# Kernel tuning notes

Measured on AMD Instinct MI355X. Metric: run time of the kernel, lower is better.

## Reference

```python
import jax, jax.numpy as jnp
import numpy as np

NH, DH, DHR = 16, 128, 64  # heads, head dim, decoupled rope dim
ROPE_BASE = 10000.0

def _rope(x):
    # x: (B, L, H, Dr) with Dr even; interleaved-pair RoPE (torchtune style)
    B, L, H, Dr = x.shape
    pos = jnp.arange(L, dtype=jnp.float32)
    inv_freq = 1.0 / (ROPE_BASE ** (jnp.arange(0, Dr, 2, dtype=jnp.float32) / Dr))
    ang = pos[:, None] * inv_freq[None, :]          # (L, Dr/2)
    cos = jnp.cos(ang)[None, :, None, :].astype(x.dtype)
    sin = jnp.sin(ang)[None, :, None, :].astype(x.dtype)
    x1, x2 = x[..., 0::2], x[..., 1::2]
    out = jnp.stack([x1 * cos - x2 * sin, x1 * sin + x2 * cos], axis=-1)
    return out.reshape(B, L, H, Dr)

def setup_inputs() -> dict:
    key = jax.random.key(0)
    ks = jax.random.split(key, 9)
    s = 0.02
    return {
        'x':     jax.random.normal(ks[0], (2, 2048, 2048), jnp.float32),
        'W_DKV': jax.random.normal(ks[1], (2048, 682), jnp.float32) * s,
        'W_UK':  jax.random.normal(ks[2], (682, 2048), jnp.float32) * s,
        'W_UV':  jax.random.normal(ks[3], (682, 2048), jnp.float32) * s,
        'W_KR':  jax.random.normal(ks[4], (2048, 64), jnp.float32) * s,
        'W_DQ':  jax.random.normal(ks[5], (2048, 682), jnp.float32) * s,
        'W_UQ':  jax.random.normal(ks[6], (682, 2048), jnp.float32) * s,
        'W_QR':  jax.random.normal(ks[7], (682, 1024), jnp.float32) * s,
        'W_O':   jax.random.normal(ks[8], (2048, 2048), jnp.float32) * s,
    }

def reference(x, W_DKV, W_UK, W_UV, W_KR, W_DQ, W_UQ, W_QR, W_O):
    B, L, D = x.shape
    # --- KV path ---
    c_KV = x @ W_DKV                                   # (B, L, dc)
    k_C = (c_KV @ W_UK).reshape(B, L, NH, DH)          # content keys
    k_R = _rope((x @ W_KR).reshape(B, L, 1, DHR))      # shared rope key head
    k_R = jnp.broadcast_to(k_R, (B, L, NH, DHR))
    k = jnp.concatenate([k_C, k_R], axis=-1)           # (B, L, NH, DH+DHR)
    v = (c_KV @ W_UV).reshape(B, L, NH, DH)
    # --- Q path ---
    c_Q = x @ W_DQ                                     # (B, L, dc')
    q_C = (c_Q @ W_UQ).reshape(B, L, NH, DH)
    q_R = _rope((c_Q @ W_QR).reshape(B, L, NH, DHR))
    q = jnp.concatenate([q_C, q_R], axis=-1)           # (B, L, NH, DH+DHR)
    # --- attention (causal) ---
    scale = 1.0 / jnp.sqrt(jnp.float32(DH + DHR))
    scores = jnp.einsum('blhd,bmhd->bhlm', q, k) * scale
    causal = jnp.tril(jnp.ones((L, L), dtype=bool))
    scores = jnp.where(causal[None, None], scores, jnp.finfo(scores.dtype).min)
    attn = jax.nn.softmax(scores, axis=-1)
    o = jnp.einsum('bhlm,bmhd->blhd', attn, v).reshape(B, L, NH * DH)
    return o @ W_O
```

## Files before the change

kernel.cpp:

```cpp
#include <hip/hip_runtime.h>
#include <stdint.h>

typedef __attribute__((ext_vector_type(8))) __bf16 bf16x8;
typedef __attribute__((ext_vector_type(4))) float f32x4;

#define DEVI static __device__ __forceinline__

DEVI uint16_t f2b(float f) {
  uint32_t u = __float_as_uint(f);
  u += 0x7FFFu + ((u >> 16) & 1u);
  return (uint16_t)(u >> 16);
}
DEVI float b2f(uint16_t b) { return __uint_as_float(((uint32_t)b) << 16); }

DEVI void gl_lds16(const void* g, void* l) {
  __builtin_amdgcn_global_load_lds((const __attribute__((address_space(1))) void*)g,
                                   (__attribute__((address_space(3))) void*)l, 16, 0, 0);
}

DEVI f32x4 mfma16(bf16x8 a, bf16x8 b, f32x4 c) {
  return __builtin_amdgcn_mfma_f32_16x16x32_bf16(a, b, c, 0, 0, 0);
}

#define BARX asm volatile("s_barrier" ::: "memory")
#define WLG0 asm volatile("s_waitcnt lgkmcnt(0)" ::: "memory")
#define WV4 asm volatile("s_waitcnt vmcnt(4)" ::: "memory")
#define PRIO1 __builtin_amdgcn_s_setprio(1)
#define PRIO0 __builtin_amdgcn_s_setprio(0)

static constexpr size_t OFF_XB = 0;
static constexpr size_t OFF_WD = 8388608;
static constexpr size_t OFF_WUKV = OFF_WD + 3670016;
static constexpr size_t OFF_WUQR = OFF_WUKV + 3145728;
static constexpr size_t OFF_WO = OFF_WUQR + 2359296;
static constexpr size_t OFF_CD = OFF_WO + 4194304;
static constexpr size_t OFF_CUKV = OFF_CD + 7340032;
static constexpr size_t OFF_CUQR = OFF_CUKV + 16777216;
static constexpr size_t OFF_VT = OFF_CUQR + 12582912;

__global__ void pre_kernel(const float* __restrict__ x, const float* __restrict__ Wdkv,
                           const float* __restrict__ Wuk, const float* __restrict__ Wuv,
                           const float* __restrict__ Wkr, const float* __restrict__ Wdq,
                           const float* __restrict__ Wuq, const float* __restrict__ Wqr,
                           const float* __restrict__ Wo, uint16_t* __restrict__ ws) {
  const int bid = blockIdx.x;
  const int t = threadIdx.x;
  if (bid >= 3264) {
    int id = (bid - 3264) * 256 + t;
    float4 v = ((const float4*)x)[id];
    uint16_t o[4] = {f2b(v.x), f2b(v.y), f2b(v.z), f2b(v.w)};
    *(uint64_t*)&ws[OFF_XB + (size_t)id * 4] = *(uint64_t*)o;
    return;
  }
  const float* W;
  uint16_t* Wt;
  int Kw, Nw, Kp, nx, rb;
  if (bid < 384) {
    W = Wdkv; Wt = ws + OFF_WD; Kw = 2048; Nw = 682; Kp = 2048; nx = 12; rb = bid;
  } else if (bid < 768) {
    W = Wdq; Wt = ws + OFF_WD + (size_t)768 * 2048; Kw = 2048; Nw = 682; Kp = 2048; nx = 12; rb = bid - 384;
  } else if (bid < 896) {
    W = Wkr; Wt = ws + OFF_WD + (size_t)1536 * 2048; Kw = 2048; Nw = 64; Kp = 2048; nx = 4; rb = bid - 768;
  } else if (bid < 1280) {
    W = Wuk; Wt = ws + OFF_WUKV; Kw = 682; Nw = 2048; Kp = 768; nx = 32; rb = bid - 896;
  } else if (bid < 1664) {
    W = Wuv; Wt = ws + OFF_WUKV + (size_t)2048 * 768; Kw = 682; Nw = 2048; Kp = 768; nx = 32; rb = bid - 1280;
  } else if (bid < 2048) {
    W = Wuq; Wt = ws + OFF_WUQR; Kw = 682; Nw = 2048; Kp = 768; nx = 32; rb = bid - 1664;
  } else if (bid < 2240) {
    W = Wqr; Wt = ws + OFF_WUQR + (size_t)2048 * 768; Kw = 682; Nw = 1024; Kp = 768; nx = 16; rb = bid - 2048;
  } else {
    W = Wo; Wt = ws + OFF_WO; Kw = 2048; Nw = 2048; Kp = 2048; nx = 32; rb = bid - 2240;
  }
  const int n0 = (rb % nx) * 64, k0 = (rb / nx) * 64;
  __shared__ uint16_t T[64][72];
#pragma unroll
  for (int p = 0; p < 2; ++p) {
    int r = p * 32 + (t >> 3);
    int c0 = (t & 7) * 8;
    int gr = k0 + r;
#pragma unroll
    for (int e = 0; e < 8; ++e) {
      int gc = n0 + c0 + e;
      float v = (gr < Kw && gc < Nw) ? W[(size_t)gr * Nw + gc] : 0.f;
      T[c0 + e][r] = f2b(v);
    }
  }
  __syncthreads();
#pragma unroll
  for (int p = 0; p < 2; ++p) {
    int dr = p * 32 + (t >> 3);
    int mc = (t & 7) * 8;
    uint16_t tmp[8];
#pragma unroll
    for (int e = 0; e < 8; ++e) tmp[e] = T[dr][mc + e];
    *(uint64_t*)&Wt[(size_t)(n0 + dr) * Kp + k0 + mc] = ((uint64_t*)tmp)[0];
    *(uint64_t*)&Wt[(size_t)(n0 + dr) * Kp + k0 + mc + 4] = ((uint64_t*)tmp)[1];
  }
}

template <int BM, bool F32OUT>
__global__ __launch_bounds__(512, 2) void gemm8(const uint16_t* __restrict__ A, int lda,
                                                const uint16_t* __restrict__ Bt,
                                                void* __restrict__ Cv, int ldc, int K) {
  constexpr int MF = BM / 32;
  constexpr int MH = MF / 2;
  constexpr int AL = BM / 128;
  constexpr int ABYTES = BM * 128;
  __shared__ char lds[2 * BM * 128 + 2 * 256 * 128];
  char* const LB = lds + 2 * ABYTES;
  const int tid = threadIdx.x;
  const int lane = tid & 63;
  const int lr = lane & 15, lgb = (lane >> 4) * 16;
  const int wid = tid >> 6;
  const int g = wid >> 2;
  const int wc = (wid & 3) * 64;
  const int rA0 = g * (BM / 2) + lr;
  const int rB0 = wc + lr;
  const size_t row0 = (size_t)blockIdx.y * BM, col0 = (size_t)blockIdx.x * 256;
  const char* Agb = (const char*)(A + row0 * lda);
  const char* Btb = (const char*)(Bt + col0 * K);
  const size_t ldab = (size_t)lda * 2;
  const size_t ldbb = (size_t)K * 2;
  const int nk = K >> 6;
  const int ni = nk >> 1;

  f32x4 acc[MF][4] = {};
  bf16x8 aF[MH][2], bF[4][2];

  auto stageA = [&](int kt, int buf, int hf) {
#pragma unroll
    for (int j = 0; j < AL; ++j) {
      int c = j * 512 + tid;
      int cl = c ^ (((c >> 5) & 1) << 1);
      int row = hf * (BM / 2) + (cl >> 3);
      gl_lds16(Agb + (size_t)row * ldab + (size_t)kt * 128 + (cl & 7) * 16,
               lds + buf * ABYTES + hf * (ABYTES / 2) + (j * 512 + (tid & 0x1C0)) * 16);
    }
  };
  auto stageB = [&](int kt, int buf, int hf) {
#pragma unroll
    for (int j = 0; j < 2; ++j) {
      int c = j * 512 + tid;
      int cl = c ^ (((c >> 5) & 1) << 1);
      int row = hf * 128 + (cl >> 3);
      gl_lds16(Btb + (size_t)row * ldbb + (size_t)kt * 128 + (cl & 7) * 16,
               LB + buf * 32768 + hf * 16384 + (j * 512 + (tid & 0x1C0)) * 16);
    }
  };
  auto ldAm = [&](int buf, int mb) {
#pragma unroll
    for (int m = 0; m < MH; ++m) {
      int r = rA0 + (mb + m) * 16;
      int ro = r * 128;
      int sw = ((r >> 2) & 1) << 5;
#pragma unroll
      for (int kk = 0; kk < 2; ++kk)
        aF[m][kk] = *(const bf16x8*)(lds + buf * ABYTES + ((ro + kk * 64 + lgb) ^ sw));
    }
  };
  auto ldBn = [&](int buf, int nb) {
#pragma unroll
    for (int n = 0; n < 2; ++n) {
      int r = rB0 + (nb + n) * 16;
      int ro = r * 128;
      int sw = ((r >> 2) & 1) << 5;
#pragma unroll
      for (int kk = 0; kk < 2; ++kk)
        bF[nb + n][kk] = *(const bf16x8*)(LB + buf * 32768 + ((ro + kk * 64 + lgb) ^ sw));
    }
  };
  auto mmac = [&](int mb, int nb) {
#pragma unroll
    for (int m = 0; m < MH; ++m)
#pragma unroll
      for (int n = 0; n < 2; ++n)
#pragma unroll
        for (int kk = 0; kk < 2; ++kk)
          acc[mb + m][nb + n] = mfma16(aF[m][kk], bF[nb + n][kk], acc[mb + m][nb + n]);
  };

  stageA(0, 0, 0); stageA(0, 0, 1); stageB(0, 0, 0); stageB(0, 0, 1);
  stageB(1, 1, 0); stageB(1, 1, 1);
  WV4; BARX;

  for (int i = 0; i < ni; ++i) {
    const int t1 = 2 * i + 1;
    const int tn = (2 * i + 2 < nk) ? 2 * i + 2 : nk - 1;
    const int tn1 = (2 * i + 3 < nk) ? 2 * i + 3 : nk - 1;
    ldAm(0, 0); ldBn(0, 0); stageA(t1, 1, 0);
    BARX; WLG0; PRIO1; mmac(0, 0); PRIO0; BARX;
    ldBn(0, 2); stageA(t1, 1, 1);
    BARX; WLG0; PRIO1; mmac(0, 2); PRIO0; BARX;
    ldAm(0, MH); stageB(tn, 0, 0);
    BARX; WLG0; PRIO1; mmac(MH, 0); PRIO0; BARX;
    stageB(tn, 0, 1);
    BARX; PRIO1; mmac(MH, 2); PRIO0; WV4; BARX;
    ldAm(1, 0); ldBn(1, 0); stageA(tn, 0, 0);
    BARX; WLG0; PRIO1; mmac(0, 0); PRIO0; BARX;
    ldBn(1, 2); stageA(tn, 0, 1);
    BARX; WLG0; PRIO1; mmac(0, 2); PRIO0; BARX;
    ldAm(1, MH); stageB(tn1, 1, 0);
    BARX; WLG0; PRIO1; mmac(MH, 0); PRIO0; BARX;
    stageB(tn1, 1, 1);
    BARX; PRIO1; mmac(MH, 2); PRIO0; WV4; BARX;
  }
  asm volatile("s_waitcnt vmcnt(0)" ::: "memory");

#pragma unroll
  for (int m = 0; m < MF; ++m)
#pragma unroll
    for (int n = 0; n < 4; ++n)
#pragma unroll
      for (int j = 0; j < 4; ++j) {
        size_t row = row0 + g * (BM / 2) + m * 16 + (lane >> 4) * 4 + j;
        size_t col = col0 + wc + n * 16 + lr;
        if (F32OUT)
          ((float*)Cv)[row * ldc + col] = acc[m][n][j];
        else
          ((uint16_t*)Cv)[row * ldc + col] = f2b(acc[m][n][j]);
      }
}

__global__ void rope_k_kernel(uint16_t* __restrict__ cd) {
  int id = blockIdx.x * 256 + threadIdx.x;
  int row = id >> 5, i = id & 31;
  int pos = row & 2047;
  float invf = exp2f(-13.287712379549449f * (float)i / 32.f);
  float ang = (float)pos * invf;
  float s, c;
  sincosf(ang, &s, &c);
  size_t base = (size_t)row * 1792 + 1536 + 2 * i;
  float x1 = b2f(cd[base]), x2 = b2f(cd[base + 1]);
  cd[base] = f2b(x1 * c - x2 * s);
  cd[base + 1] = f2b(x1 * s + x2 * c);
}

__global__ void rope_q_kernel(uint16_t* __restrict__ cu) {
  int id = blockIdx.x * 256 + threadIdx.x;
  int row = id >> 9;
  int rem = id & 511;
  int h = rem >> 5, i = rem & 31;
  int pos = row & 2047;
  float invf = exp2f(-13.287712379549449f * (float)i / 32.f);
  float ang = (float)pos * invf;
  float s, c;
  sincosf(ang, &s, &c);
  size_t base = (size_t)row * 3072 + 2048 + h * 64 + 2 * i;
  float x1 = b2f(cu[base]), x2 = b2f(cu[base + 1]);
  cu[base] = f2b(x1 * c - x2 * s);
  cu[base + 1] = f2b(x1 * s + x2 * c);
}

__global__ void vtrans_kernel(const uint16_t* __restrict__ v, uint16_t* __restrict__ vt) {
  __shared__ uint16_t T[64][72];
  const int t = threadIdx.x;
  const int mt = blockIdx.x, dt = blockIdx.y, bh = blockIdx.z;
  const int b = bh >> 4, h = bh & 15;
  const int m0 = mt * 64, d0 = dt * 64;
#pragma unroll
  for (int p = 0; p < 2; ++p) {
    int r = p * 32 + (t >> 3), c8 = (t & 7) * 8;
    const uint16_t* s = &v[((size_t)(b * 2048 + m0 + r)) * 4096 + 2048 + h * 128 + d0 + c8];
    uint16_t tmp[8];
    ((uint64_t*)tmp)[0] = ((const uint64_t*)s)[0];
    ((uint64_t*)tmp)[1] = ((const uint64_t*)s)[1];
#pragma unroll
    for (int e = 0; e < 8; ++e) T[c8 + e][r] = tmp[e];
  }
  __syncthreads();
#pragma unroll
  for (int p = 0; p < 2; ++p) {
    int dr = p * 32 + (t >> 3), mc = (t & 7) * 8;
    uint16_t tmp[8];
#pragma unroll
    for (int e = 0; e < 8; ++e) tmp[e] = T[dr][mc + e];
    uint16_t* dstp = &vt[((size_t)(bh * 128 + d0 + dr)) * 2048 + m0 + mc];
    ((uint64_t*)dstp)[0] = ((uint64_t*)tmp)[0];
    ((uint64_t*)dstp)[1] = ((uint64_t*)tmp)[1];
  }
}

__global__ __launch_bounds__(512, 2) void attn_kernel(const uint16_t* __restrict__ cuqr,
                                                      const uint16_t* __restrict__ cukv,
                                                      const uint16_t* __restrict__ cd,
                                                      const uint16_t* __restrict__ vt,
                                                      uint16_t* __restrict__ obuf) {
  __shared__ uint16_t Ks[64 * 192];
  __shared__ uint16_t Vs[128 * 64];
  __shared__ uint16_t Ps[8 * 16 * 64];
  const int tid = threadIdx.x;
  const int wid = tid >> 6, lane = tid & 63;
  const int lr = lane & 15, lg = lane >> 4;
  const int bid = blockIdx.x;
  const int wg = (bid & 7) * 32 + (bid >> 3);
  const int pairi = wg & 7;
  const int bh = wg >> 3;
  const int b = bh >> 4, h = bh & 15;
  const float sc2 = 0.07216878364870323f * 1.4426950408889634f;

  const char* Kcb = (const char*)cukv + (size_t)b * 2048 * 8192 + h * 256;
  const char* Krb = (const char*)cd + (size_t)b * 2048 * 3584 + 3072;
  const char* Vb = (const char*)vt + (size_t)bh * 524288;
  char* KsB = (char*)Ks;
  char* VsB = (char*)Vs;
  char* PwB = (char*)(Ps + wid * 1024);

  const char* kbase[3];
  size_t kstep[3];
  int klds[3];
#pragma unroll
  for (int i = 0; i < 3; ++i) {
    int c = i * 512 + tid;
    int r = c / 24, c16 = c % 24;
    klds[i] = r * 384 + ((c16 * 16) ^ ((r & 7) << 4));
    if (c16 < 16) {
      kbase[i] = Kcb + (size_t)r * 8192 + c16 * 16;
      kstep[i] = (size_t)64 * 8192;
    } else {
      kbase[i] = Krb + (size_t)r * 3584 + (c16 - 16) * 16;
      kstep[i] = (size_t)64 * 3584;
    }
  }
  const char* vbase[2];
  int vlds[2];
#pragma unroll
  for (int i = 0; i < 2; ++i) {
    int c = i * 512 + tid;
    int d = c >> 3, c16 = c & 7;
    vlds[i] = d * 128 + ((c16 * 16) ^ ((d & 7) << 4));
    vbase[i] = Vb + (size_t)d * 4096 + c16 * 16;
  }

  for (int ph = 0; ph < 2; ++ph) {
    const int qt = ph ? (15 - pairi) : pairi;
    const int q0 = qt * 128;
    const int nt = 2 * (qt + 1);
    const int qrow = q0 + wid * 16 + lr;
    bf16x8 qf[6];
    {
      const char* Qcp = (const char*)cuqr + (size_t)(b * 2048 + qrow) * 6144 + h * 256 + lg * 16;
      const char* Qrp =
          (const char*)cuqr + (size_t)(b * 2048 + qrow) * 6144 + 4096 + h * 128 + lg * 16;
#pragma unroll
      for (int kb = 0; kb < 4; ++kb) qf[kb] = *(const bf16x8*)(Qcp + kb * 64);
#pragma unroll
      for (int kb = 0; kb < 2; ++kb) qf[4 + kb] = *(const bf16x8*)(Qrp + kb * 64);
    }
    f32x4 o[8] = {};
    float mrun[4], lrun[4];
#pragma unroll
    for (int j = 0; j < 4; ++j) { mrun[j] = -INFINITY; lrun[j] = 0.f; }

    const char* kp[3];
    const char* vp[2];
    bf16x8 kreg[3], vreg[2];
#pragma unroll
    for (int i = 0; i < 3; ++i) kp[i] = kbase[i];
#pragma unroll
    for (int i = 0; i < 2; ++i) vp[i] = vbase[i];
#pragma unroll
    for (int i = 0; i < 3; ++i) { kreg[i] = *(const bf16x8*)kp[i]; kp[i] += kstep[i]; }
#pragma unroll
    for (int i = 0; i < 2; ++i) { vreg[i] = *(const bf16x8*)vp[i]; vp[i] += 128; }
#pragma unroll
    for (int i = 0; i < 3; ++i) *(bf16x8*)(KsB + klds[i]) = kreg[i];
#pragma unroll
    for (int i = 0; i < 2; ++i) *(bf16x8*)(VsB + vlds[i]) = vreg[i];
    __syncthreads();

    for (int t = 0; t < nt; ++t) {
      const bool more = (t + 1 < nt);
      if (more) {
#pragma unroll
        for (int i = 0; i < 3; ++i) { kreg[i] = *(const bf16x8*)kp[i]; kp[i] += kstep[i]; }
#pragma unroll
        for (int i = 0; i < 2; ++i) { vreg[i] = *(const bf16x8*)vp[i]; vp[i] += 128; }
      }
      if (t * 64 <= q0 + wid * 16 + 15) {
        f32x4 s[4] = {};
        __builtin_amdgcn_s_setprio(1);
#pragma unroll
        for (int n = 0; n < 4; ++n) {
          int r = n * 16 + lr;
          const char* kptr = KsB + r * 384;
          int sw = (r & 7) << 4;
#pragma unroll
          for (int kb = 0; kb < 6; ++kb)
            s[n] = mfma16(qf[kb], *(const bf16x8*)(kptr + ((kb * 64 + lg * 16) ^ sw)), s[n]);
        }
        __builtin_amdgcn_s_setprio(0);
        if (t * 64 + 63 > q0 + wid * 16) {
#pragma unroll
          for (int n = 0; n < 4; ++n)
#pragma unroll
            for (int j = 0; j < 4; ++j)
              if (t * 64 + n * 16 + lr > q0 + wid * 16 + lg * 4 + j) s[n][j] = -INFINITY;
        }
        float pm[4];
#pragma unroll
        for (int j = 0; j < 4; ++j) {
          float v = fmaxf(fmaxf(s[0][j], s[1][j]), fmaxf(s[2][j], s[3][j]));
          v = fmaxf(v, __shfl_xor(v, 1));
          v = fmaxf(v, __shfl_xor(v, 2));
          v = fmaxf(v, __shfl_xor(v, 4));
          v = fmaxf(v, __shfl_xor(v, 8));
          pm[j] = v;
        }
        bool exceed = false;
#pragma unroll
        for (int j = 0; j < 4; ++j) exceed |= (pm[j] > mrun[j] + 76.8f);
        if (__any(exceed)) {
          float alpha[4];
#pragma unroll
          for (int j = 0; j < 4; ++j) {
            float mn = fmaxf(mrun[j], pm[j]);
            alpha[j] = exp2f((mrun[j] - mn) * sc2);
            mrun[j] = mn;
            lrun[j] *= alpha[j];
          }
#pragma unroll
          for (int n2 = 0; n2 < 8; ++n2)
#pragma unroll
            for (int j = 0; j < 4; ++j) o[n2][j] *= alpha[j];
        }
        float rs[4] = {0.f, 0.f, 0.f, 0.f};
#pragma unroll
        for (int n = 0; n < 4; ++n)
#pragma unroll
          for (int j = 0; j < 4; ++j) {
            float p = exp2f((s[n][j] - mrun[j]) * sc2);
            rs[j] += p;
            int row = lg * 4 + j;
            *(uint16_t*)(PwB + row * 128 + ((((n * 16 + lr)) * 2) ^ ((row & 7) << 4))) = f2b(p);
          }
#pragma unroll
        for (int j = 0; j < 4; ++j) {
          float v = rs[j];
          v += __shfl_xor(v, 1);
          v += __shfl_xor(v, 2);
          v += __shfl_xor(v, 4);
          v += __shfl_xor(v, 8);
          lrun[j] += v;
        }
        __builtin_amdgcn_s_setprio(1);
#pragma unroll
        for (int kb2 = 0; kb2 < 2; ++kb2) {
          bf16x8 pa = *(const bf16x8*)(PwB + lr * 128 + ((kb2 * 64 + lg * 16) ^ ((lr & 7) << 4)));
#pragma unroll
          for (int n2 = 0; n2 < 8; ++n2) {
            int vr = n2 * 16 + lr;
            o[n2] = mfma16(
                pa, *(const bf16x8*)(VsB + vr * 128 + ((kb2 * 64 + lg * 16) ^ ((vr & 7) << 4))),
                o[n2]);
          }
        }
        __builtin_amdgcn_s_setprio(0);
      }
      __syncthreads();
      if (more) {
#pragma unroll
        for (int i = 0; i < 3; ++i) *(bf16x8*)(KsB + klds[i]) = kreg[i];
#pragma unroll
        for (int i = 0; i < 2; ++i) *(bf16x8*)(VsB + vlds[i]) = vreg[i];
        __syncthreads();
      }
    }
    float inv[4];
#pragma unroll
    for (int j = 0; j < 4; ++j) inv[j] = 1.f / lrun[j];
#pragma unroll
    for (int n2 = 0; n2 < 8; ++n2)
#pragma unroll
      for (int j = 0; j < 4; ++j) {
        size_t row = (size_t)b * 2048 + q0 + wid * 16 + lg * 4 + j;
        size_t col = (size_t)h * 128 + n2 * 16 + lr;
        obuf[row * 2048 + col] = f2b(o[n2][j] * inv[j]);
      }
  }
}

extern "C" void kernel_launch(void* const* d_in, const int* in_sizes, int n_in,
                              void* d_out, int out_size, void* d_ws, size_t ws_size,
                              hipStream_t stream) {
  (void)in_sizes; (void)n_in; (void)out_size; (void)ws_size;
  const float* x = (const float*)d_in[0];
  const float* Wdkv = (const float*)d_in[1];
  const float* Wuk = (const float*)d_in[2];
  const float* Wuv = (const float*)d_in[3];
  const float* Wkr = (const float*)d_in[4];
  const float* Wdq = (const float*)d_in[5];
  const float* Wuq = (const float*)d_in[6];
  const float* Wqr = (const float*)d_in[7];
  const float* Wo = (const float*)d_in[8];
  uint16_t* ws = (uint16_t*)d_ws;

  uint16_t* xb = ws + OFF_XB;
  uint16_t* obuf = ws + OFF_XB;
  uint16_t* wd = ws + OFF_WD;
  uint16_t* wukv = ws + OFF_WUKV;
  uint16_t* wuqr = ws + OFF_WUQR;
  uint16_t* wo = ws + OFF_WO;
  uint16_t* cd = ws + OFF_CD;
  uint16_t* cukv = ws + OFF_CUKV;
  uint16_t* cuqr = ws + OFF_CUQR;
  uint16_t* vtb = ws + OFF_VT;

  pre_kernel<<<11456, 256, 0, stream>>>(x, Wdkv, Wuk, Wuv, Wkr, Wdq, Wuq, Wqr, Wo, ws);
  gemm8<128, false><<<dim3(7, 32), 512, 0, stream>>>(xb, 2048, wd, cd, 1792, 2048);
  gemm8<256, false><<<dim3(16, 16), 512, 0, stream>>>(cd, 1792, wukv, cukv, 4096, 768);
  gemm8<256, false><<<dim3(12, 16), 512, 0, stream>>>(cd + 768, 1792, wuqr, cuqr, 3072, 768);
  rope_k_kernel<<<512, 256, 0, stream>>>(cd);
  rope_q_kernel<<<8192, 256, 0, stream>>>(cuqr);
  vtrans_kernel<<<dim3(32, 2, 32), 256, 0, stream>>>(cukv, vtb);
  attn_kernel<<<256, 512, 0, stream>>>(cuqr, cukv, cd, vtb, obuf);
  gemm8<128, true><<<dim3(8, 32), 512, 0, stream>>>(obuf, 2048, wo, d_out, 2048, 2048);
}
```

Before: 279.8 us.

## Double-buffer attention K/V tiles, defer row-sum reduction, merge rope/transpose kernels

Attention K/V shared-memory tiles become double-buffered, so the next tile is written into the alternate buffer before a single barrier per iteration, replacing the two barriers used before. The per-tile cross-lane shuffle reduction of the softmax row sum is moved to one reduction after the loop; this relies on the per-lane partial sums being rescaled consistently by the same alpha. The two RoPE kernels and the V transpose kernel are merged into one launch to cut launch overhead. Shared memory per block grows, which may limit occupancy at the 2-blocks-per-CU launch bound.

```diff
diff --git a/kernel.cpp b/kernel.cpp
--- a/kernel.cpp
+++ b/kernel.cpp
@@ -222,46 +222,49 @@
       }
 }
 
-__global__ void rope_k_kernel(uint16_t* __restrict__ cd) {
-  int id = blockIdx.x * 256 + threadIdx.x;
-  int row = id >> 5, i = id & 31;
-  int pos = row & 2047;
-  float invf = exp2f(-13.287712379549449f * (float)i / 32.f);
-  float ang = (float)pos * invf;
-  float s, c;
-  sincosf(ang, &s, &c);
-  size_t base = (size_t)row * 1792 + 1536 + 2 * i;
-  float x1 = b2f(cd[base]), x2 = b2f(cd[base + 1]);
-  cd[base] = f2b(x1 * c - x2 * s);
-  cd[base + 1] = f2b(x1 * s + x2 * c);
-}
-
-__global__ void rope_q_kernel(uint16_t* __restrict__ cu) {
-  int id = blockIdx.x * 256 + threadIdx.x;
-  int row = id >> 9;
-  int rem = id & 511;
-  int h = rem >> 5, i = rem & 31;
-  int pos = row & 2047;
-  float invf = exp2f(-13.287712379549449f * (float)i / 32.f);
-  float ang = (float)pos * invf;
-  float s, c;
-  sincosf(ang, &s, &c);
-  size_t base = (size_t)row * 3072 + 2048 + h * 64 + 2 * i;
-  float x1 = b2f(cu[base]), x2 = b2f(cu[base + 1]);
-  cu[base] = f2b(x1 * c - x2 * s);
-  cu[base + 1] = f2b(x1 * s + x2 * c);
-}
-
-__global__ void vtrans_kernel(const uint16_t* __restrict__ v, uint16_t* __restrict__ vt) {
-  __shared__ uint16_t T[64][72];
+__global__ void misc_kernel(uint16_t* __restrict__ cd, uint16_t* __restrict__ cuqr,
+                            const uint16_t* __restrict__ cukv, uint16_t* __restrict__ vt) {
+  const int bid = blockIdx.x;
   const int t = threadIdx.x;
-  const int mt = blockIdx.x, dt = blockIdx.y, bh = blockIdx.z;
+  if (bid < 512) {
+    int id = bid * 256 + t;
+    int row = id >> 5, i = id & 31;
+    int pos = row & 2047;
+    float invf = exp2f(-13.287712379549449f * (float)i / 32.f);
+    float ang = (float)pos * invf;
+    float s, c;
+    sincosf(ang, &s, &c);
+    size_t base = (size_t)row * 1792 + 1536 + 2 * i;
+    float x1 = b2f(cd[base]), x2 = b2f(cd[base + 1]);
+    cd[base] = f2b(x1 * c - x2 * s);
+    cd[base + 1] = f2b(x1 * s + x2 * c);
+    return;
+  }
+  if (bid < 8704) {
+    int id = (bid - 512) * 256 + t;
+    int row = id >> 9;
+    int rem = id & 511;
+    int h = rem >> 5, i = rem & 31;
+    int pos = row & 2047;
+    float invf = exp2f(-13.287712379549449f * (float)i / 32.f);
+    float ang = (float)pos * invf;
+    float s, c;
+    sincosf(ang, &s, &c);
+    size_t base = (size_t)row * 3072 + 2048 + h * 64 + 2 * i;
+    float x1 = b2f(cuqr[base]), x2 = b2f(cuqr[base + 1]);
+    cuqr[base] = f2b(x1 * c - x2 * s);
+    cuqr[base + 1] = f2b(x1 * s + x2 * c);
+    return;
+  }
+  const int idx = bid - 8704;
+  const int mt = idx & 31, dt = (idx >> 5) & 1, bh = idx >> 6;
   const int b = bh >> 4, h = bh & 15;
   const int m0 = mt * 64, d0 = dt * 64;
+  __shared__ uint16_t T[64][72];
 #pragma unroll
   for (int p = 0; p < 2; ++p) {
     int r = p * 32 + (t >> 3), c8 = (t & 7) * 8;
-    const uint16_t* s = &v[((size_t)(b * 2048 + m0 + r)) * 4096 + 2048 + h * 128 + d0 + c8];
+    const uint16_t* s = &cukv[((size_t)(b * 2048 + m0 + r)) * 4096 + 2048 + h * 128 + d0 + c8];
     uint16_t tmp[8];
     ((uint64_t*)tmp)[0] = ((const uint64_t*)s)[0];
     ((uint64_t*)tmp)[1] = ((const uint64_t*)s)[1];
@@ -286,8 +289,8 @@
                                                       const uint16_t* __restrict__ cd,
                                                       const uint16_t* __restrict__ vt,
                                                       uint16_t* __restrict__ obuf) {
-  __shared__ uint16_t Ks[64 * 192];
-  __shared__ uint16_t Vs[128 * 64];
+  __shared__ uint16_t Ks[2][64 * 192];
+  __shared__ uint16_t Vs[2][128 * 64];
   __shared__ uint16_t Ps[8 * 16 * 64];
   const int tid = threadIdx.x;
   const int wid = tid >> 6, lane = tid & 63;
@@ -302,8 +305,8 @@
   const char* Kcb = (const char*)cukv + (size_t)b * 2048 * 8192 + h * 256;
   const char* Krb = (const char*)cd + (size_t)b * 2048 * 3584 + 3072;
   const char* Vb = (const char*)vt + (size_t)bh * 524288;
-  char* KsB = (char*)Ks;
-  char* VsB = (char*)Vs;
+  char* const Ks0 = (char*)Ks[0];
+  char* const Vs0 = (char*)Vs[0];
   char* PwB = (char*)(Ps + wid * 1024);
 
   const char* kbase[3];
@@ -364,9 +367,9 @@
 #pragma unroll
     for (int i = 0; i < 2; ++i) { vreg[i] = *(const bf16x8*)vp[i]; vp[i] += 128; }
 #pragma unroll
-    for (int i = 0; i < 3; ++i) *(bf16x8*)(KsB + klds[i]) = kreg[i];
-#pragma unroll
-    for (int i = 0; i < 2; ++i) *(bf16x8*)(VsB + vlds[i]) = vreg[i];
+    for (int i = 0; i < 3; ++i) *(bf16x8*)(Ks0 + klds[i]) = kreg[i];
+#pragma unroll
+    for (int i = 0; i < 2; ++i) *(bf16x8*)(Vs0 + vlds[i]) = vreg[i];
     __syncthreads();
 
     for (int t = 0; t < nt; ++t) {
@@ -377,6 +380,9 @@
 #pragma unroll
         for (int i = 0; i < 2; ++i) { vreg[i] = *(const bf16x8*)vp[i]; vp[i] += 128; }
       }
+      const int cb = t & 1;
+      const char* KsB = Ks0 + cb * 24576;
+      const char* VsB = Vs0 + cb * 16384;
       if (t * 64 <= q0 + wid * 16 + 15) {
         f32x4 s[4] = {};
         __builtin_amdgcn_s_setprio(1);
@@ -435,14 +441,7 @@
             *(uint16_t*)(PwB + row * 128 + ((((n * 16 + lr)) * 2) ^ ((row & 7) << 4))) = f2b(p);
           }
 #pragma unroll
-        for (int j = 0; j < 4; ++j) {
-          float v = rs[j];
-          v += __shfl_xor(v, 1);
-          v += __shfl_xor(v, 2);
-          v += __shfl_xor(v, 4);
-          v += __shfl_xor(v, 8);
-          lrun[j] += v;
-        }
+        for (int j = 0; j < 4; ++j) lrun[j] += rs[j];
         __builtin_amdgcn_s_setprio(1);
 #pragma unroll
         for (int kb2 = 0; kb2 < 2; ++kb2) {
@@ -457,14 +456,24 @@
         }
         __builtin_amdgcn_s_setprio(0);
       }
+      if (more) {
+        char* KsN = Ks0 + (cb ^ 1) * 24576;
+        char* VsN = Vs0 + (cb ^ 1) * 16384;
+#pragma unroll
+        for (int i = 0; i < 3; ++i) *(bf16x8*)(KsN + klds[i]) = kreg[i];
+#pragma unroll
+        for (int i = 0; i < 2; ++i) *(bf16x8*)(VsN + vlds[i]) = vreg[i];
+      }
       __syncthreads();
-      if (more) {
-#pragma unroll
-        for (int i = 0; i < 3; ++i) *(bf16x8*)(KsB + klds[i]) = kreg[i];
-#pragma unroll
-        for (int i = 0; i < 2; ++i) *(bf16x8*)(VsB + vlds[i]) = vreg[i];
-        __syncthreads();
-      }
+    }
+#pragma unroll
+    for (int j = 0; j < 4; ++j) {
+      float v = lrun[j];
+      v += __shfl_xor(v, 1);
+      v += __shfl_xor(v, 2);
+      v += __shfl_xor(v, 4);
+      v += __shfl_xor(v, 8);
+      lrun[j] = v;
     }
     float inv[4];
 #pragma unroll
@@ -510,9 +519,7 @@
   gemm8<128, false><<<dim3(7, 32), 512, 0, stream>>>(xb, 2048, wd, cd, 1792, 2048);
   gemm8<256, false><<<dim3(16, 16), 512, 0, stream>>>(cd, 1792, wukv, cukv, 4096, 768);
   gemm8<256, false><<<dim3(12, 16), 512, 0, stream>>>(cd + 768, 1792, wuqr, cuqr, 3072, 768);
-  rope_k_kernel<<<512, 256, 0, stream>>>(cd);
-  rope_q_kernel<<<8192, 256, 0, stream>>>(cuqr);
-  vtrans_kernel<<<dim3(32, 2, 32), 256, 0, stream>>>(cukv, vtb);
+  misc_kernel<<<10752, 256, 0, stream>>>(cd, cuqr, cukv, vtb);
   attn_kernel<<<256, 512, 0, stream>>>(cuqr, cukv, cd, vtb, obuf);
   gemm8<128, true><<<dim3(8, 32), 512, 0, stream>>>(obuf, 2048, wo, d_out, 2048, 2048);
 }
```

New measurement: 265.3 us (median of 2 runs). -5.2%, faster.
